# Kernel optimization log

Measured on AMD Instinct MI355X. Metric: run time of the kernel, lower is better.

The kernel has to match this reference:

```python
import jax, jax.numpy as jnp
import numpy as np

N_HEADS = 16
ROPE_THETA = 10000.0


def _rope_cos_sin(seq_len, head_dim):
    # freqs for pairs (2i, 2i+1): [seq_len, head_dim//2]
    inv_freq = 1.0 / (ROPE_THETA ** (jnp.arange(0, head_dim, 2, dtype=jnp.float32) / head_dim))
    angles = jnp.arange(seq_len, dtype=jnp.float32)[:, None] * inv_freq[None, :]
    return jnp.cos(angles), jnp.sin(angles)


def _apply_rope(t, cos, sin):
    # t: [B, H, S, hd]; complex multiply on interleaved pairs
    tr = t.reshape(*t.shape[:-1], -1, 2)  # [B,H,S,hd//2,2]
    x0, x1 = tr[..., 0], tr[..., 1]
    r0 = x0 * cos - x1 * sin
    r1 = x0 * sin + x1 * cos
    return jnp.stack([r0, r1], axis=-1).reshape(t.shape)


def setup_inputs() -> dict:
    key = jax.random.key(0)
    ks = jax.random.split(key, 5)
    B, S, D = 2, 2048, 2048
    scale = 0.02
    return {
        "x": jax.random.normal(ks[0], (B, S, D), jnp.float32),
        "wq": jax.random.normal(ks[1], (D, D), jnp.float32) * scale,
        "wk": jax.random.normal(ks[2], (D, D), jnp.float32) * scale,
        "wv": jax.random.normal(ks[3], (D, D), jnp.float32) * scale,
        "wo": jax.random.normal(ks[4], (D, D), jnp.float32) * scale,
    }


def reference(x, wq, wk, wv, wo):
    B, S, D = x.shape
    H = N_HEADS
    hd = D // H
    # QKV projections (Linear with no bias: x @ W.T), split heads -> [B,H,S,hd]
    def proj(w):
        return jnp.einsum('bsd,ed->bse', x, w).reshape(B, S, H, hd).transpose(0, 2, 1, 3)
    q, k, v = proj(wq), proj(wk), proj(wv)
    cos, sin = _rope_cos_sin(S, hd)  # [S, hd//2] each
    cos = cos[None, None]            # [1,1,S,hd//2]
    sin = sin[None, None]
    q = _apply_rope(q, cos, sin)
    k = _apply_rope(k, cos, sin)
    # causal SDPA
    scores = jnp.einsum('bhqd,bhkd->bhqk', q, k) / jnp.sqrt(jnp.float32(hd))
    causal = jnp.tril(jnp.ones((S, S), dtype=bool))
    scores = jnp.where(causal, scores, jnp.finfo(scores.dtype).min)
    attn = jax.nn.softmax(scores, axis=-1)
    out = jnp.einsum('bhqk,bhkd->bhqd', attn, v)
    out = out.transpose(0, 2, 1, 3).reshape(B, S, D)
    return jnp.einsum('bsd,ed->bse', out, wo)
```

## Files before the change

kernel.cpp:

```cpp
#include <hip/hip_runtime.h>
#include <stdint.h>

typedef __attribute__((ext_vector_type(4))) float f32x4;
typedef __attribute__((ext_vector_type(8))) short short8;
typedef __attribute__((ext_vector_type(4))) short s16x4;

#define DEV __device__ __forceinline__

constexpr int Bc = 2, Sc = 2048, Dc = 2048, Hc = 16, HDc = 128;
constexpr int Mc = Bc * Sc;
constexpr float ATTN_SCALE = 0.08838834764831843f;

DEV short f2bf(float f) {
  unsigned u = __float_as_uint(f);
  unsigned r = (u + 0x7fffu + ((u >> 16) & 1u)) >> 16;
  return (short)(unsigned short)r;
}

DEV void gload_lds16(const void* gsrc, void* ldst) {
  typedef const __attribute__((address_space(1))) void as1_cvoid;
  typedef __attribute__((address_space(3))) void as3_void;
  __builtin_amdgcn_global_load_lds((as1_cvoid*)(uintptr_t)gsrc,
                                   (as3_void*)(uint32_t)(uintptr_t)ldst,
                                   16, 0, 0);
}

__global__ void cast_f32_bf16(const float* __restrict__ in, short* __restrict__ out, int n8) {
  int i = blockIdx.x * 256 + threadIdx.x;
  if (i >= n8) return;
  f32x4 a = ((const f32x4*)in)[i * 2];
  f32x4 b = ((const f32x4*)in)[i * 2 + 1];
  short8 o;
  o[0] = f2bf(a[0]); o[1] = f2bf(a[1]); o[2] = f2bf(a[2]); o[3] = f2bf(a[3]);
  o[4] = f2bf(b[0]); o[5] = f2bf(b[1]); o[6] = f2bf(b[2]); o[7] = f2bf(b[3]);
  ((short8*)out)[i] = o;
}

__global__ void rope_table(float* __restrict__ ct, float* __restrict__ st) {
  int t = blockIdx.x * 256 + threadIdx.x;
  int s = t >> 6, i = t & 63;
  float freq = powf(10000.0f, -(float)(2 * i) * (1.0f / 128.0f));
  float a = (float)s * freq;
  float sv, cv;
  sincosf(a, &sv, &cv);
  ct[t] = cv; st[t] = sv;
}

__global__ __launch_bounds__(256) void gemm_qkv(
    const short* __restrict__ A,
    const short* __restrict__ Wq, const short* __restrict__ Wk, const short* __restrict__ Wv,
    short* __restrict__ qo, short* __restrict__ ko, short* __restrict__ vo,
    const float* __restrict__ ct, const float* __restrict__ st) {
  constexpr int K = Dc;
  __shared__ short Al[128 * 32];
  __shared__ short Bl[128 * 32];
  const int tid = threadIdx.x, lane = tid & 63, w = tid >> 6;
  const int g = lane >> 4, c = lane & 15;
  const int wr = w >> 1, wc = w & 1;
  const int m0 = blockIdx.y * 128;
  const int n0 = blockIdx.x * 128;
  const int which = n0 >> 11;
  const int wn0 = n0 & (Dc - 1);
  const short* W = (which == 0) ? Wq : (which == 1) ? Wk : Wv;

  f32x4 acc[4][4] = {};

  const int cid = w * 64 + lane;
  const short* a0 = A + (size_t)(m0 + (cid >> 2)) * K + (cid & 3) * 8;
  const short* a1 = A + (size_t)(m0 + 64 + (cid >> 2)) * K + (cid & 3) * 8;
  const short* b0 = W + (size_t)(wn0 + (cid >> 2)) * K + (cid & 3) * 8;
  const short* b1 = W + (size_t)(wn0 + 64 + (cid >> 2)) * K + (cid & 3) * 8;
  char* lA0 = (char*)Al + w * 1024;
  char* lA1 = (char*)Al + 4096 + w * 1024;
  char* lB0 = (char*)Bl + w * 1024;
  char* lB1 = (char*)Bl + 4096 + w * 1024;

  for (int kt = 0; kt < K / 32; ++kt) {
    const int ko_ = kt * 32;
    gload_lds16(a0 + ko_, lA0);
    gload_lds16(a1 + ko_, lA1);
    gload_lds16(b0 + ko_, lB0);
    gload_lds16(b1 + ko_, lB1);
    __syncthreads();
    short8 af[4], wf[4];
#pragma unroll
    for (int fi = 0; fi < 4; ++fi)
      af[fi] = *(const short8*)&Al[(wr * 64 + fi * 16 + c) * 32 + g * 8];
#pragma unroll
    for (int fj = 0; fj < 4; ++fj)
      wf[fj] = *(const short8*)&Bl[(wc * 64 + fj * 16 + c) * 32 + g * 8];
#pragma unroll
    for (int fi = 0; fi < 4; ++fi)
#pragma unroll
      for (int fj = 0; fj < 4; ++fj)
        acc[fi][fj] = __builtin_amdgcn_mfma_f32_16x16x32_bf16(af[fi], wf[fj], acc[fi][fj], 0, 0, 0);
    __syncthreads();
  }

  if (which < 2) {
    short* outb = (which == 0) ? qo : ko;
#pragma unroll
    for (int fi = 0; fi < 4; ++fi)
#pragma unroll
      for (int fj = 0; fj < 4; ++fj)
#pragma unroll
        for (int r = 0; r < 4; ++r) {
          int row = m0 + wr * 64 + fi * 16 + g * 4 + r;
          int col = wn0 + wc * 64 + fj * 16 + c;
          float v = acc[fi][fj][r];
          float other = __shfl_xor(v, 1);
          int pi = (col & (HDc - 1)) >> 1;
          int sp = row & (Sc - 1);
          float cv = ct[sp * 64 + pi], sv = st[sp * 64 + pi];
          v = ((col & 1) == 0) ? (v * cv - other * sv) : (other * sv + v * cv);
          int b_ = row >> 11, sq = row & (Sc - 1);
          int h_ = col >> 7, dd = col & (HDc - 1);
          outb[((size_t)(b_ * Hc + h_) * Sc + sq) * HDc + dd] = f2bf(v);
        }
  } else {
#pragma unroll
    for (int fi = 0; fi < 4; ++fi)
#pragma unroll
      for (int fj = 0; fj < 4; ++fj) {
        int row0 = m0 + wr * 64 + fi * 16 + g * 4;
        int col = wn0 + wc * 64 + fj * 16 + c;
        int b_ = row0 >> 11, sq0 = row0 & (Sc - 1);
        int h_ = col >> 7, dd = col & (HDc - 1);
        s16x4 pk;
#pragma unroll
        for (int r = 0; r < 4; ++r) pk[r] = f2bf(acc[fi][fj][r]);
        *(s16x4*)&vo[((size_t)(b_ * Hc + h_) * HDc + dd) * Sc + sq0] = pk;
      }
  }
}

__global__ __launch_bounds__(256) void gemm_out(
    const short* __restrict__ A, const short* __restrict__ W, float* __restrict__ outf) {
  constexpr int K = Dc;
  __shared__ short Al[128 * 32];
  __shared__ short Bl[128 * 32];
  const int tid = threadIdx.x, lane = tid & 63, w = tid >> 6;
  const int g = lane >> 4, c = lane & 15;
  const int wr = w >> 1, wc = w & 1;
  const int m0 = blockIdx.y * 128, n0 = blockIdx.x * 128;

  f32x4 acc[4][4] = {};
  const int cid = w * 64 + lane;
  const short* a0 = A + (size_t)(m0 + (cid >> 2)) * K + (cid & 3) * 8;
  const short* a1 = A + (size_t)(m0 + 64 + (cid >> 2)) * K + (cid & 3) * 8;
  const short* b0 = W + (size_t)(n0 + (cid >> 2)) * K + (cid & 3) * 8;
  const short* b1 = W + (size_t)(n0 + 64 + (cid >> 2)) * K + (cid & 3) * 8;
  char* lA0 = (char*)Al + w * 1024;
  char* lA1 = (char*)Al + 4096 + w * 1024;
  char* lB0 = (char*)Bl + w * 1024;
  char* lB1 = (char*)Bl + 4096 + w * 1024;

  for (int kt = 0; kt < K / 32; ++kt) {
    const int ko_ = kt * 32;
    gload_lds16(a0 + ko_, lA0);
    gload_lds16(a1 + ko_, lA1);
    gload_lds16(b0 + ko_, lB0);
    gload_lds16(b1 + ko_, lB1);
    __syncthreads();
    short8 af[4], wf[4];
#pragma unroll
    for (int fi = 0; fi < 4; ++fi)
      af[fi] = *(const short8*)&Al[(wr * 64 + fi * 16 + c) * 32 + g * 8];
#pragma unroll
    for (int fj = 0; fj < 4; ++fj)
      wf[fj] = *(const short8*)&Bl[(wc * 64 + fj * 16 + c) * 32 + g * 8];
#pragma unroll
    for (int fi = 0; fi < 4; ++fi)
#pragma unroll
      for (int fj = 0; fj < 4; ++fj)
        acc[fi][fj] = __builtin_amdgcn_mfma_f32_16x16x32_bf16(af[fi], wf[fj], acc[fi][fj], 0, 0, 0);
    __syncthreads();
  }

#pragma unroll
  for (int fi = 0; fi < 4; ++fi)
#pragma unroll
    for (int fj = 0; fj < 4; ++fj)
#pragma unroll
      for (int r = 0; r < 4; ++r) {
        int row = m0 + wr * 64 + fi * 16 + g * 4 + r;
        int col = n0 + wc * 64 + fj * 16 + c;
        outf[(size_t)row * Dc + col] = acc[fi][fj][r];
      }
}

DEV void stage_kv(const short* kh, const short* vth, int kv0,
                  short* Kb, short* Vb, int w, int tid) {
#pragma unroll
  for (int i = 0; i < 4; ++i) {
    int L = i * 256 + tid;
    int row = L >> 4, p = L & 15;
    gload_lds16(kh + (size_t)(kv0 + row) * HDc + ((p ^ (row & 7)) * 8),
                (char*)Kb + i * 4096 + w * 1024);
  }
#pragma unroll
  for (int i = 0; i < 4; ++i) {
    int L = i * 256 + tid;
    int row = L >> 3, p = L & 7;
    gload_lds16(vth + (size_t)row * Sc + kv0 + ((p ^ (row & 7)) * 8),
                (char*)Vb + i * 4096 + w * 1024);
  }
}

__global__ __launch_bounds__(256) void attn_kernel(
    const short* __restrict__ qb, const short* __restrict__ kb,
    const short* __restrict__ vtb, short* __restrict__ ob) {
  __shared__ short Kl[2][64 * 128];
  __shared__ short Vl[2][128 * 64];
  __shared__ short Pl[4 * 16 * 72];

  const int tid = threadIdx.x, lane = tid & 63, w = tid >> 6;
  const int g = lane >> 4, c = lane & 15;
  const int bh = blockIdx.y;
  const int b_ = bh >> 4, h_ = bh & 15;
  const short* qh = qb + (size_t)bh * Sc * HDc;
  const short* kh = kb + (size_t)bh * Sc * HDc;
  const short* vth = vtb + (size_t)bh * HDc * Sc;

  for (int pass = 0; pass < 2; ++pass) {
    const int qt = pass ? (31 - blockIdx.x) : blockIdx.x;
    const int q0 = qt * 64;

    short8 qf[4];
#pragma unroll
    for (int kc = 0; kc < 4; ++kc)
      qf[kc] = *(const short8*)&qh[(size_t)(q0 + w * 16 + c) * HDc + kc * 32 + g * 8];

    float mrow[4], lrow[4];
    f32x4 acc[8] = {};
#pragma unroll
    for (int r = 0; r < 4; ++r) { mrow[r] = -1e30f; lrow[r] = 0.f; }

    const int nt = qt + 1;
    int cur = 0;
    stage_kv(kh, vth, 0, Kl[0], Vl[0], w, tid);
    __syncthreads();

    for (int kvt = 0; kvt < nt; ++kvt) {
      if (kvt + 1 < nt)
        stage_kv(kh, vth, (kvt + 1) * 64, Kl[cur ^ 1], Vl[cur ^ 1], w, tid);

      f32x4 sacc[4];
#pragma unroll
      for (int kb_ = 0; kb_ < 4; ++kb_) {
        sacc[kb_] = (f32x4){0.f, 0.f, 0.f, 0.f};
#pragma unroll
        for (int kc = 0; kc < 4; ++kc) {
          short8 kf = *(const short8*)&Kl[cur][(kb_ * 16 + c) * 128 + (((kc * 4 + g) ^ (c & 7)) * 8)];
          sacc[kb_] = __builtin_amdgcn_mfma_f32_16x16x32_bf16(qf[kc], kf, sacc[kb_], 0, 0, 0);
        }
      }
      float p[4][4];
      const bool last = (kvt == qt);
      const int kv0 = kvt * 64;
#pragma unroll
      for (int kb_ = 0; kb_ < 4; ++kb_)
#pragma unroll
        for (int r = 0; r < 4; ++r) {
          float s = sacc[kb_][r] * ATTN_SCALE;
          if (last) {
            int qg = q0 + w * 16 + g * 4 + r;
            int kg = kv0 + kb_ * 16 + c;
            if (kg > qg) s = -1e30f;
          }
          p[kb_][r] = s;
        }
      float scal[4];
#pragma unroll
      for (int r = 0; r < 4; ++r) {
        float v = fmaxf(fmaxf(p[0][r], p[1][r]), fmaxf(p[2][r], p[3][r]));
        v = fmaxf(v, __shfl_xor(v, 1));
        v = fmaxf(v, __shfl_xor(v, 2));
        v = fmaxf(v, __shfl_xor(v, 4));
        v = fmaxf(v, __shfl_xor(v, 8));
        float mn = fmaxf(mrow[r], v);
        scal[r] = __expf(mrow[r] - mn);
        mrow[r] = mn;
      }
#pragma unroll
      for (int r = 0; r < 4; ++r) {
        float acc_s = 0.f;
#pragma unroll
        for (int kb_ = 0; kb_ < 4; ++kb_) {
          p[kb_][r] = __expf(p[kb_][r] - mrow[r]);
          acc_s += p[kb_][r];
        }
        acc_s += __shfl_xor(acc_s, 1);
        acc_s += __shfl_xor(acc_s, 2);
        acc_s += __shfl_xor(acc_s, 4);
        acc_s += __shfl_xor(acc_s, 8);
        lrow[r] = lrow[r] * scal[r] + acc_s;
      }
#pragma unroll
      for (int db = 0; db < 8; ++db)
#pragma unroll
        for (int r = 0; r < 4; ++r) acc[db][r] *= scal[r];
#pragma unroll
      for (int kb_ = 0; kb_ < 4; ++kb_)
#pragma unroll
        for (int r = 0; r < 4; ++r)
          Pl[w * 16 * 72 + (g * 4 + r) * 72 + kb_ * 16 + c] = f2bf(p[kb_][r]);
      short8 pa[2];
#pragma unroll
      for (int k2 = 0; k2 < 2; ++k2)
        pa[k2] = *(const short8*)&Pl[w * 16 * 72 + c * 72 + k2 * 32 + g * 8];
#pragma unroll
      for (int db = 0; db < 8; ++db)
#pragma unroll
        for (int k2 = 0; k2 < 2; ++k2) {
          short8 vf = *(const short8*)&Vl[cur][(db * 16 + c) * 64 + (((k2 * 4 + g) ^ (c & 7)) * 8)];
          acc[db] = __builtin_amdgcn_mfma_f32_16x16x32_bf16(pa[k2], vf, acc[db], 0, 0, 0);
        }
      __syncthreads();
      cur ^= 1;
    }

#pragma unroll
    for (int db = 0; db < 8; ++db)
#pragma unroll
      for (int r = 0; r < 4; ++r) {
        int qg = q0 + w * 16 + g * 4 + r;
        int d = db * 16 + c;
        float v = acc[db][r] / lrow[r];
        ob[((size_t)(b_ * Sc + qg)) * Dc + h_ * HDc + d] = f2bf(v);
      }
  }
}

extern "C" void kernel_launch(void* const* d_in, const int* in_sizes, int n_in,
                              void* d_out, int out_size, void* d_ws, size_t ws_size,
                              hipStream_t stream) {
  const float* x = (const float*)d_in[0];
  const float* wq = (const float*)d_in[1];
  const float* wk = (const float*)d_in[2];
  const float* wv = (const float*)d_in[3];
  const float* wo = (const float*)d_in[4];
  float* out = (float*)d_out;

  char* ws = (char*)d_ws;
  short* xb  = (short*)(ws + 0);
  short* wqb = (short*)(ws + 16777216);
  short* wkb = (short*)(ws + 25165824);
  short* wvb = (short*)(ws + 33554432);
  short* wob = (short*)(ws + 41943040);
  short* qb  = (short*)(ws + 50331648);
  short* kbf = (short*)(ws + 67108864);
  short* vtb = (short*)(ws + 83886080);
  float* ct  = (float*)(ws + 100663296);
  float* st  = (float*)(ws + 101187584);
  short* obuf = xb;

  cast_f32_bf16<<<Mc * Dc / 8 / 256, 256, 0, stream>>>(x, xb, Mc * Dc / 8);
  cast_f32_bf16<<<Dc * Dc / 8 / 256, 256, 0, stream>>>(wq, wqb, Dc * Dc / 8);
  cast_f32_bf16<<<Dc * Dc / 8 / 256, 256, 0, stream>>>(wk, wkb, Dc * Dc / 8);
  cast_f32_bf16<<<Dc * Dc / 8 / 256, 256, 0, stream>>>(wv, wvb, Dc * Dc / 8);
  cast_f32_bf16<<<Dc * Dc / 8 / 256, 256, 0, stream>>>(wo, wob, Dc * Dc / 8);
  rope_table<<<Sc * 64 / 256, 256, 0, stream>>>(ct, st);

  gemm_qkv<<<dim3(3 * Dc / 128, Mc / 128), 256, 0, stream>>>(xb, wqb, wkb, wvb, qb, kbf, vtb, ct, st);

  attn_kernel<<<dim3(Sc / 128, Bc * Hc), 256, 0, stream>>>(qb, kbf, vtb, obuf);

  gemm_out<<<dim3(Dc / 128, Mc / 128), 256, 0, stream>>>(obuf, wob, out);
}
```

Baseline: 433.6 us.

## Rewrite projection GEMMs with double-buffered LDS pipeline and larger tiles

Replaces the two single-buffered 128x128 GEMM kernels with one templated kernel. It uses 512 threads, 128x256 tiles, a K-step of 64, XOR-swizzled LDS, and a two-stage double-buffered global-to-LDS pipeline with explicit waitcnt and barriers. It also remaps workgroups through a grid swizzle so neighbouring blocks share weight panels in L2, and raises MFMA priority during compute. The aim is to hide global load latency, cut barriers per K step and avoid LDS bank conflicts. In exchange it uses more LDS (96 KB per block) and fewer blocks, and the hand-placed waitcnt counts risk correctness if they are miscounted.

Result: faster. 397.1 us (-8.4%).

```diff
diff --git a/kernel.cpp b/kernel.cpp
--- a/kernel.cpp
+++ b/kernel.cpp
@@ -46,147 +46,147 @@
   ct[t] = cv; st[t] = sv;
 }
 
-__global__ __launch_bounds__(256) void gemm_qkv(
+template <int EPI>
+__global__ __launch_bounds__(512, 2) void gemm_pipe(
     const short* __restrict__ A,
-    const short* __restrict__ Wq, const short* __restrict__ Wk, const short* __restrict__ Wv,
+    const short* __restrict__ W0, const short* __restrict__ W1, const short* __restrict__ W2,
     short* __restrict__ qo, short* __restrict__ ko, short* __restrict__ vo,
+    float* __restrict__ outf,
     const float* __restrict__ ct, const float* __restrict__ st) {
-  constexpr int K = Dc;
-  __shared__ short Al[128 * 32];
-  __shared__ short Bl[128 * 32];
+  constexpr int K = Dc, NT = K / 64;
+  __shared__ short As[2][128][64];
+  __shared__ short Bs[2][2][128][64];
+
   const int tid = threadIdx.x, lane = tid & 63, w = tid >> 6;
   const int g = lane >> 4, c = lane & 15;
-  const int wr = w >> 1, wc = w & 1;
-  const int m0 = blockIdx.y * 128;
-  const int n0 = blockIdx.x * 128;
-  const int which = n0 >> 11;
-  const int wn0 = n0 & (Dc - 1);
-  const short* W = (which == 0) ? Wq : (which == 1) ? Wk : Wv;
+  const int wr = w >> 2, wc = w & 3;
+
+  const int nx = gridDim.x;
+  const int nwg = nx * gridDim.y;
+  const int flat = blockIdx.y * nx + blockIdx.x;
+  const int swz = (flat & 7) * (nwg >> 3) + (flat >> 3);
+  const int nbx = swz % nx, nby = swz / nx;
+
+  const int m0 = nby * 128;
+  const int which = (EPI == 0) ? (nbx >> 3) : 0;
+  const int wn0 = (EPI == 0) ? ((nbx & 7) * 256) : (nbx * 256);
+  const short* W = (EPI == 1) ? W0 : ((which == 0) ? W0 : (which == 1) ? W1 : W2);
+
+  const int r1 = tid >> 3, p1 = tid & 7;
+  const int psw = (p1 ^ (r1 & 7)) * 8;
+  const short* gA0 = A + (size_t)(m0 + r1) * K + psw;
+  const short* gA1 = gA0 + (size_t)64 * K;
+  const short* gB0 = W + (size_t)(wn0 + r1) * K + psw;
+  const short* gB1 = gB0 + (size_t)64 * K;
+  const short* gB2 = gB0 + (size_t)128 * K;
+  const short* gB3 = gB0 + (size_t)192 * K;
+  char* ldsA = (char*)As + w * 1024;
+  char* ldsB = (char*)Bs + w * 1024;
+
+#define STAGE(t, db)                                        \
+  do {                                                      \
+    const size_t ko_ = (size_t)(t) * 64;                    \
+    gload_lds16(gA0 + ko_, ldsA + (db) * 16384);            \
+    gload_lds16(gA1 + ko_, ldsA + (db) * 16384 + 8192);     \
+    gload_lds16(gB0 + ko_, ldsB + (db) * 32768);            \
+    gload_lds16(gB1 + ko_, ldsB + (db) * 32768 + 8192);     \
+    gload_lds16(gB2 + ko_, ldsB + (db) * 32768 + 16384);    \
+    gload_lds16(gB3 + ko_, ldsB + (db) * 32768 + 24576);    \
+  } while (0)
 
   f32x4 acc[4][4] = {};
-
-  const int cid = w * 64 + lane;
-  const short* a0 = A + (size_t)(m0 + (cid >> 2)) * K + (cid & 3) * 8;
-  const short* a1 = A + (size_t)(m0 + 64 + (cid >> 2)) * K + (cid & 3) * 8;
-  const short* b0 = W + (size_t)(wn0 + (cid >> 2)) * K + (cid & 3) * 8;
-  const short* b1 = W + (size_t)(wn0 + 64 + (cid >> 2)) * K + (cid & 3) * 8;
-  char* lA0 = (char*)Al + w * 1024;
-  char* lA1 = (char*)Al + 4096 + w * 1024;
-  char* lB0 = (char*)Bl + w * 1024;
-  char* lB1 = (char*)Bl + 4096 + w * 1024;
-
-  for (int kt = 0; kt < K / 32; ++kt) {
-    const int ko_ = kt * 32;
-    gload_lds16(a0 + ko_, lA0);
-    gload_lds16(a1 + ko_, lA1);
-    gload_lds16(b0 + ko_, lB0);
-    gload_lds16(b1 + ko_, lB1);
-    __syncthreads();
-    short8 af[4], wf[4];
-#pragma unroll
-    for (int fi = 0; fi < 4; ++fi)
-      af[fi] = *(const short8*)&Al[(wr * 64 + fi * 16 + c) * 32 + g * 8];
-#pragma unroll
-    for (int fj = 0; fj < 4; ++fj)
-      wf[fj] = *(const short8*)&Bl[(wc * 64 + fj * 16 + c) * 32 + g * 8];
-#pragma unroll
-    for (int fi = 0; fi < 4; ++fi)
-#pragma unroll
-      for (int fj = 0; fj < 4; ++fj)
-        acc[fi][fj] = __builtin_amdgcn_mfma_f32_16x16x32_bf16(af[fi], wf[fj], acc[fi][fj], 0, 0, 0);
-    __syncthreads();
-  }
-
-  if (which < 2) {
-    short* outb = (which == 0) ? qo : ko;
-#pragma unroll
-    for (int fi = 0; fi < 4; ++fi)
-#pragma unroll
-      for (int fj = 0; fj < 4; ++fj)
+  const int cx = (g ^ (c & 7)) * 16;
+  const char* aBase = (const char*)As + (wr * 64 + c) * 128;
+  const char* bBase = (const char*)Bs + (wc >> 1) * 16384 + ((wc & 1) * 64 + c) * 128;
+
+  STAGE(0, 0);
+  STAGE(1, 1);
+  asm volatile("s_waitcnt vmcnt(6)" ::: "memory");
+  __builtin_amdgcn_sched_barrier(0);
+  __builtin_amdgcn_s_barrier();
+
+  for (int t = 0; t < NT; ++t) {
+    const int db = t & 1;
+    short8 af[2][4], bf[2][4];
+    const char* aB = aBase + db * 16384;
+    const char* bB = bBase + db * 32768;
+#pragma unroll
+    for (int kk = 0; kk < 2; ++kk) {
+      const int co = cx ^ (kk * 64);
+#pragma unroll
+      for (int mi = 0; mi < 4; ++mi) af[kk][mi] = *(const short8*)(aB + mi * 2048 + co);
+#pragma unroll
+      for (int nj = 0; nj < 4; ++nj) bf[kk][nj] = *(const short8*)(bB + nj * 2048 + co);
+    }
+    asm volatile("s_waitcnt lgkmcnt(0)" ::: "memory");
+    __builtin_amdgcn_sched_barrier(0);
+    __builtin_amdgcn_s_barrier();
+    __builtin_amdgcn_sched_barrier(0);
+    if (t + 2 < NT) STAGE(t + 2, db);
+    __builtin_amdgcn_s_setprio(1);
+#pragma unroll
+    for (int kk = 0; kk < 2; ++kk)
+#pragma unroll
+      for (int mi = 0; mi < 4; ++mi)
+#pragma unroll
+        for (int nj = 0; nj < 4; ++nj)
+          acc[mi][nj] = __builtin_amdgcn_mfma_f32_16x16x32_bf16(af[kk][mi], bf[kk][nj], acc[mi][nj], 0, 0, 0);
+    __builtin_amdgcn_s_setprio(0);
+    if (t + 2 < NT) { asm volatile("s_waitcnt vmcnt(6)" ::: "memory"); }
+    else            { asm volatile("s_waitcnt vmcnt(0)" ::: "memory"); }
+    __builtin_amdgcn_sched_barrier(0);
+    __builtin_amdgcn_s_barrier();
+  }
+#undef STAGE
+
+  if constexpr (EPI == 0) {
+    if (which < 2) {
+      short* outb = (which == 0) ? qo : ko;
+#pragma unroll
+      for (int mi = 0; mi < 4; ++mi)
+#pragma unroll
+        for (int nj = 0; nj < 4; ++nj)
+#pragma unroll
+          for (int r = 0; r < 4; ++r) {
+            int row = m0 + wr * 64 + mi * 16 + g * 4 + r;
+            int col = wn0 + wc * 64 + nj * 16 + c;
+            float v = acc[mi][nj][r];
+            float other = __shfl_xor(v, 1);
+            int pi = (col & (HDc - 1)) >> 1;
+            int sp = row & (Sc - 1);
+            float cv = ct[sp * 64 + pi], sv = st[sp * 64 + pi];
+            v = ((col & 1) == 0) ? (v * cv - other * sv) : (other * sv + v * cv);
+            int b_ = row >> 11, sq = row & (Sc - 1);
+            int h_ = col >> 7, dd = col & (HDc - 1);
+            outb[((size_t)(b_ * Hc + h_) * Sc + sq) * HDc + dd] = f2bf(v);
+          }
+    } else {
+#pragma unroll
+      for (int mi = 0; mi < 4; ++mi)
+#pragma unroll
+        for (int nj = 0; nj < 4; ++nj) {
+          int row0 = m0 + wr * 64 + mi * 16 + g * 4;
+          int col = wn0 + wc * 64 + nj * 16 + c;
+          int b_ = row0 >> 11, sq0 = row0 & (Sc - 1);
+          int h_ = col >> 7, dd = col & (HDc - 1);
+          s16x4 pk;
+#pragma unroll
+          for (int r = 0; r < 4; ++r) pk[r] = f2bf(acc[mi][nj][r]);
+          *(s16x4*)&vo[((size_t)(b_ * Hc + h_) * HDc + dd) * Sc + sq0] = pk;
+        }
+    }
+  } else {
+#pragma unroll
+    for (int mi = 0; mi < 4; ++mi)
+#pragma unroll
+      for (int nj = 0; nj < 4; ++nj)
 #pragma unroll
         for (int r = 0; r < 4; ++r) {
-          int row = m0 + wr * 64 + fi * 16 + g * 4 + r;
-          int col = wn0 + wc * 64 + fj * 16 + c;
-          float v = acc[fi][fj][r];
-          float other = __shfl_xor(v, 1);
-          int pi = (col & (HDc - 1)) >> 1;
-          int sp = row & (Sc - 1);
-          float cv = ct[sp * 64 + pi], sv = st[sp * 64 + pi];
-          v = ((col & 1) == 0) ? (v * cv - other * sv) : (other * sv + v * cv);
-          int b_ = row >> 11, sq = row & (Sc - 1);
-          int h_ = col >> 7, dd = col & (HDc - 1);
-          outb[((size_t)(b_ * Hc + h_) * Sc + sq) * HDc + dd] = f2bf(v);
-        }
-  } else {
-#pragma unroll
-    for (int fi = 0; fi < 4; ++fi)
-#pragma unroll
-      for (int fj = 0; fj < 4; ++fj) {
-        int row0 = m0 + wr * 64 + fi * 16 + g * 4;
-        int col = wn0 + wc * 64 + fj * 16 + c;
-        int b_ = row0 >> 11, sq0 = row0 & (Sc - 1);
-        int h_ = col >> 7, dd = col & (HDc - 1);
-        s16x4 pk;
-#pragma unroll
-        for (int r = 0; r < 4; ++r) pk[r] = f2bf(acc[fi][fj][r]);
-        *(s16x4*)&vo[((size_t)(b_ * Hc + h_) * HDc + dd) * Sc + sq0] = pk;
-      }
-  }
-}
-
-__global__ __launch_bounds__(256) void gemm_out(
-    const short* __restrict__ A, const short* __restrict__ W, float* __restrict__ outf) {
-  constexpr int K = Dc;
-  __shared__ short Al[128 * 32];
-  __shared__ short Bl[128 * 32];
-  const int tid = threadIdx.x, lane = tid & 63, w = tid >> 6;
-  const int g = lane >> 4, c = lane & 15;
-  const int wr = w >> 1, wc = w & 1;
-  const int m0 = blockIdx.y * 128, n0 = blockIdx.x * 128;
-
-  f32x4 acc[4][4] = {};
-  const int cid = w * 64 + lane;
-  const short* a0 = A + (size_t)(m0 + (cid >> 2)) * K + (cid & 3) * 8;
-  const short* a1 = A + (size_t)(m0 + 64 + (cid >> 2)) * K + (cid & 3) * 8;
-  const short* b0 = W + (size_t)(n0 + (cid >> 2)) * K + (cid & 3) * 8;
-  const short* b1 = W + (size_t)(n0 + 64 + (cid >> 2)) * K + (cid & 3) * 8;
-  char* lA0 = (char*)Al + w * 1024;
-  char* lA1 = (char*)Al + 4096 + w * 1024;
-  char* lB0 = (char*)Bl + w * 1024;
-  char* lB1 = (char*)Bl + 4096 + w * 1024;
-
-  for (int kt = 0; kt < K / 32; ++kt) {
-    const int ko_ = kt * 32;
-    gload_lds16(a0 + ko_, lA0);
-    gload_lds16(a1 + ko_, lA1);
-    gload_lds16(b0 + ko_, lB0);
-    gload_lds16(b1 + ko_, lB1);
-    __syncthreads();
-    short8 af[4], wf[4];
-#pragma unroll
-    for (int fi = 0; fi < 4; ++fi)
-      af[fi] = *(const short8*)&Al[(wr * 64 + fi * 16 + c) * 32 + g * 8];
-#pragma unroll
-    for (int fj = 0; fj < 4; ++fj)
-      wf[fj] = *(const short8*)&Bl[(wc * 64 + fj * 16 + c) * 32 + g * 8];
-#pragma unroll
-    for (int fi = 0; fi < 4; ++fi)
-#pragma unroll
-      for (int fj = 0; fj < 4; ++fj)
-        acc[fi][fj] = __builtin_amdgcn_mfma_f32_16x16x32_bf16(af[fi], wf[fj], acc[fi][fj], 0, 0, 0);
-    __syncthreads();
-  }
-
-#pragma unroll
-  for (int fi = 0; fi < 4; ++fi)
-#pragma unroll
-    for (int fj = 0; fj < 4; ++fj)
-#pragma unroll
-      for (int r = 0; r < 4; ++r) {
-        int row = m0 + wr * 64 + fi * 16 + g * 4 + r;
-        int col = n0 + wc * 64 + fj * 16 + c;
-        outf[(size_t)row * Dc + col] = acc[fi][fj][r];
-      }
+          int row = m0 + wr * 64 + mi * 16 + g * 4 + r;
+          int col = wn0 + wc * 64 + nj * 16 + c;
+          outf[(size_t)row * Dc + col] = acc[mi][nj][r];
+        }
+  }
 }
 
 DEV void stage_kv(const short* kh, const short* vth, int kv0,
@@ -362,9 +362,10 @@
   cast_f32_bf16<<<Dc * Dc / 8 / 256, 256, 0, stream>>>(wo, wob, Dc * Dc / 8);
   rope_table<<<Sc * 64 / 256, 256, 0, stream>>>(ct, st);
 
-  gemm_qkv<<<dim3(3 * Dc / 128, Mc / 128), 256, 0, stream>>>(xb, wqb, wkb, wvb, qb, kbf, vtb, ct, st);
+  gemm_pipe<0><<<dim3(24, 32), 512, 0, stream>>>(xb, wqb, wkb, wvb, qb, kbf, vtb, nullptr, ct, st);
 
   attn_kernel<<<dim3(Sc / 128, Bc * Hc), 256, 0, stream>>>(qb, kbf, vtb, obuf);
 
-  gemm_out<<<dim3(Dc / 128, Mc / 128), 256, 0, stream>>>(obuf, wob, out);
-}
+  gemm_pipe<1><<<dim3(8, 32), 512, 0, stream>>>(obuf, wob, nullptr, nullptr,
+                                                nullptr, nullptr, nullptr, out, ct, st);
+}
```
